# Optimization experiments

Measured on AMD Instinct MI355X. Metric: run time of the kernel, lower is better.

Reference implementation:

```python
import jax, jax.numpy as jnp
import numpy as np

VOCAB_SIZE = 128
HIDDEN_DIM = 128
NUM_STATES = 64
STACK_VOCAB_SIZE = 32
STACK_DEPTH = 64
NUM_MEM_ACTIONS = 2 + STACK_VOCAB_SIZE  # 0=NOOP, 1=POP, k>=2 => PUSH symbol (k-2)
NUM_BUF_ACTIONS = VOCAB_SIZE
T, B = 512, 512


def setup_inputs() -> dict:
    key = jax.random.key(0)
    ks = jax.random.split(key, 10)
    return {
        "x": jax.random.randint(ks[0], (T, B), 0, VOCAB_SIZE),
        "true_act": jax.random.randint(ks[1], (T, B), 0, NUM_MEM_ACTIONS),
        "true_s": jax.random.randint(ks[2], (T, B), 0, NUM_STATES),
        "use_forcing": jax.random.randint(ks[3], (T, B), 0, 2),
        "embed": jax.random.normal(ks[4], (VOCAB_SIZE, HIDDEN_DIM), jnp.float32) * 0.02,
        "W_mem": jax.random.normal(ks[5], (HIDDEN_DIM + NUM_STATES + STACK_VOCAB_SIZE, NUM_MEM_ACTIONS), jnp.float32) * 0.05,
        "b_mem": jnp.zeros((NUM_MEM_ACTIONS,), jnp.float32),
        "W_buf": jax.random.normal(ks[6], (HIDDEN_DIM + NUM_STATES + STACK_VOCAB_SIZE, NUM_BUF_ACTIONS), jnp.float32) * 0.05,
        "b_buf": jnp.zeros((NUM_BUF_ACTIONS,), jnp.float32),
        "W_state": jax.random.normal(ks[7], (HIDDEN_DIM + NUM_STATES + STACK_VOCAB_SIZE, NUM_STATES), jnp.float32) * 0.05,
        "b_state": jnp.zeros((NUM_STATES,), jnp.float32),
    }


def update_stack(stack, ptr, action):
    # stack: [STACK_DEPTH] int, ptr: [] int, action: [] int
    is_push = action >= 2
    is_pop = action == 1
    new_ptr = jnp.clip(ptr + jnp.where(is_push, 1, 0) - jnp.where(is_pop, 1, 0), 0, STACK_DEPTH - 1)
    sym = jnp.maximum(action - 2, 0)
    stack_new = stack.at[new_ptr].set(jnp.where(is_push, sym, stack[new_ptr]))
    r_new = stack_new[new_ptr]  # read top of stack
    return stack_new, new_ptr, r_new


def reference(x, true_act, true_s, use_forcing, embed, W_mem, b_mem, W_buf, b_buf, W_state, b_state):
    def step(carry, inp):
        stack, ptr, r_prev, s_prev = carry
        x_t, t_act, t_s, forcing = inp
        x_emb = embed[x_t]                                   # [B, H] gather
        s_emb = jax.nn.one_hot(s_prev, NUM_STATES, dtype=embed.dtype)
        r_emb = jax.nn.one_hot(r_prev, STACK_VOCAB_SIZE, dtype=embed.dtype)
        flat = jnp.concatenate([x_emb, s_emb, r_emb], axis=-1)  # [B, 224]
        logits_mem = flat @ W_mem + b_mem
        logits_buf = flat @ W_buf + b_buf
        logits_state = flat @ W_state + b_state
        pred_act = jnp.argmax(logits_mem, axis=-1)
        pred_state = jnp.argmax(logits_state, axis=-1)
        action = jnp.where(forcing > 0, t_act, pred_act)
        next_s = jnp.where(forcing > 0, t_s, pred_state)
        stack_new, ptr_new, r_new = jax.vmap(update_stack)(stack, ptr, action)
        return (stack_new, ptr_new, r_new, next_s), (logits_mem, logits_buf, logits_state)

    init = (
        jnp.zeros((B, STACK_DEPTH), jnp.int32),
        jnp.zeros((B,), jnp.int32),
        jnp.zeros((B,), jnp.int32),
        jnp.zeros((B,), jnp.int32),
    )
    _, (lm, lb, ls) = jax.lax.scan(step, init, (x, true_act, true_s, use_forcing))
    return lm, lb, ls
```

## Files before the change

kernel.cpp:

```cpp
#include <hip/hip_runtime.h>
#include <stdint.h>
#include <limits.h>


#define TT 512
#define BB 512
#define HH 128
#define NSs 64
#define NMm 34
#define NBb 128

typedef unsigned short u16;
typedef float f2 __attribute__((ext_vector_type(2)));

__global__ __launch_bounds__(256) void precompute_M(
    const float* __restrict__ embed,
    const float* __restrict__ Wm, const float* __restrict__ bm,
    const float* __restrict__ Wb, const float* __restrict__ bb,
    const float* __restrict__ Ws, const float* __restrict__ bs,
    float* __restrict__ Mm32, float* __restrict__ Ms32,
    float* __restrict__ Mb32, float* __restrict__ MmT,
    float* __restrict__ MsT) {
  __shared__ double e[HH];
  const int v = blockIdx.x;
  const int tid = threadIdx.x;
  if (tid < HH) e[tid] = (double)embed[v * HH + tid];
  __syncthreads();
  if (tid < NMm) {
    const int j = tid;
    double acc = 0.0;
    for (int h = 0; h < HH; ++h) acc += e[h] * (double)Wm[h * NMm + j];
    const float r = (float)(acc + (double)bm[j]);
    Mm32[v * NMm + j] = r;
    MmT[j * 128 + v] = r;
  } else if (tid < NMm + NSs) {
    const int j = tid - NMm;
    double acc = 0.0;
    for (int h = 0; h < HH; ++h) acc += e[h] * (double)Ws[h * NSs + j];
    const float r = (float)(acc + (double)bs[j]);
    Ms32[v * NSs + j] = r;
    MsT[j * 128 + v] = r;
  } else if (tid < NMm + NSs + NBb) {
    const int j = tid - NMm - NSs;
    double acc = 0.0;
    for (int h = 0; h < HH; ++h) acc += e[h] * (double)Wb[h * NBb + j];
    Mb32[v * NBb + j] = (float)(acc + (double)bb[j]);
  }
}

__global__ __launch_bounds__(128) void build_lut(
    const float* __restrict__ Wm, const float* __restrict__ Ws,
    const float* __restrict__ MmT, const float* __restrict__ MsT,
    u16* __restrict__ lut) {
  __shared__ float wms[NMm], wmr[NMm], wss[NSs], wsr[NSs];
  const int s = blockIdx.x >> 5;
  const int r = blockIdx.x & 31;
  const int tid = threadIdx.x;
  if (tid < NMm) {
    wms[tid] = Wm[(128 + s) * NMm + tid];
    wmr[tid] = Wm[(192 + r) * NMm + tid];
  }
  if (tid < NSs) {
    wss[tid] = Ws[(128 + s) * NSs + tid];
    wsr[tid] = Ws[(192 + r) * NSs + tid];
  }
  __syncthreads();

  const int v = tid;
  int bestm = INT_MIN, act = 0;
#pragma unroll
  for (int j = 0; j < NMm; ++j) {
    const double val = (double)MmT[j * 128 + v] + (double)wms[j] + (double)wmr[j];
    const int iv = (int)(val * 67108864.0);
    if (iv > bestm) { bestm = iv; act = j; }
  }
  int bests = INT_MIN, ns = 0;
#pragma unroll
  for (int j = 0; j < NSs; ++j) {
    const double val = (double)MsT[j * 128 + v] + (double)wss[j] + (double)wsr[j];
    const int iv = (int)(val * 67108864.0);
    if (iv > bests) { bests = iv; ns = j; }
  }
  lut[(unsigned)blockIdx.x * 128 + v] = (u16)(act | (ns << 6));
}

__global__ __launch_bounds__(512, 1) void sm_fused(
    const int* __restrict__ x, const int* __restrict__ tact,
    const int* __restrict__ tstate, const int* __restrict__ forc,
    const u16* __restrict__ lut,
    const float* __restrict__ Wm, const float* __restrict__ Wb,
    const float* __restrict__ Ws,
    const float* __restrict__ Mm32, const float* __restrict__ Ms32,
    const float* __restrict__ Mb32, float* __restrict__ out) {
  __shared__ unsigned sPk[TT];
  __shared__ volatile u16 trajL[TT];
  const int tid = threadIdx.x;
  const int b = blockIdx.x;
  for (int t = tid; t < TT; t += 512) {
    const int g = t * BB + b;
    sPk[t] = (unsigned)x[g] | ((unsigned)tact[g] << 8) |
             ((unsigned)tstate[g] << 16) | ((unsigned)forc[g] << 24);
    trajL[t] = 0xFFFFu;
  }
  __syncthreads();

  const int lane = tid & 63;
  const int w = tid >> 6;

  if (w == 0) {
    __builtin_amdgcn_s_setprio(1);
    int stackv = 0;
    int ptr = 0, rr = 0, s = 0;
    unsigned p0 = sPk[0], p1 = sPk[1], p2 = sPk[2];

    for (int t = 0; t < TT; ++t) {
      const unsigned p3 = sPk[t + 3 < TT ? t + 3 : TT - 1];
      const unsigned pk_s = __builtin_amdgcn_readfirstlane(p0);

      if (lane == 0) trajL[t] = (u16)(s | (rr << 8));

      int act, ns;
      if (pk_s >> 24) {
        act = (int)((p0 >> 8) & 63u);
        ns = (int)((p0 >> 16) & 63u);
      } else {
        const int idx = s * 4096 + rr * 128 + (int)(p0 & 127u);
        const int lv = lut[idx];
        act = lv & 63;
        ns = (lv >> 6) & 63;
      }

      const bool ispush = act >= 2;
      int npn = ptr + (ispush ? 1 : 0) - (act == 1 ? 1 : 0);
      npn = npn < 0 ? 0 : (npn > 63 ? 63 : npn);
      if (ispush && lane == npn) stackv = act - 2;
      rr = __builtin_amdgcn_ds_bpermute(npn * 4, stackv);
      ptr = npn;
      s = ns;

      p0 = p1; p1 = p2; p2 = p3;
    }
  } else {
    const int j = w - 1;
    float* outLM = out;
    float* outLB = out + (size_t)TT * BB * NMm;
    float* outLS = out + (size_t)TT * BB * (NMm + NBb);

    for (int t = j; t < TT; t += 7) {
      int pr = trajL[t];
      while (pr == 0xFFFF) {
        __builtin_amdgcn_s_sleep(4);
        pr = trajL[t];
      }
      const unsigned pk = sPk[t];
      const int xv = (int)(pk & 127u);
      const int s = pr & 255;
      const int r = pr >> 8;
      const int rs = 128 + s, rr = 192 + r;
      const int row = t * BB + b;
      if (lane < NMm)
        __builtin_nontemporal_store(
            Mm32[xv * NMm + lane] + Wm[rs * NMm + lane] + Wm[rr * NMm + lane],
            &outLM[(size_t)row * NMm + lane]);
      __builtin_nontemporal_store(
          Ms32[xv * NSs + lane] + Ws[rs * NSs + lane] + Ws[rr * NSs + lane],
          &outLS[(size_t)row * NSs + lane]);
      const f2 mb  = *(const f2*)&Mb32[xv * NBb + 2 * lane];
      const f2 wbs = *(const f2*)&Wb[rs * NBb + 2 * lane];
      const f2 wbr = *(const f2*)&Wb[rr * NBb + 2 * lane];
      f2 o;
      o.x = mb.x + wbs.x + wbr.x;
      o.y = mb.y + wbs.y + wbr.y;
      __builtin_nontemporal_store(o, (f2*)&outLB[(size_t)row * NBb + 2 * lane]);
    }
  }
}

extern "C" void kernel_launch(void* const* d_in, const int* in_sizes, int n_in,
                              void* d_out, int out_size, void* d_ws, size_t ws_size,
                              hipStream_t stream) {
  if (ws_size < 690176) return;

  const int* x     = (const int*)d_in[0];
  const int* tactp = (const int*)d_in[1];
  const int* tstp  = (const int*)d_in[2];
  const int* forcp = (const int*)d_in[3];
  const float* embed = (const float*)d_in[4];
  const float* Wm = (const float*)d_in[5];
  const float* bm = (const float*)d_in[6];
  const float* Wb = (const float*)d_in[7];
  const float* bb = (const float*)d_in[8];
  const float* Ws = (const float*)d_in[9];
  const float* bs = (const float*)d_in[10];

  char* wsp = (char*)d_ws;
  float* Mm32 = (float*)(wsp);
  float* Ms32 = (float*)(wsp + 17408);
  float* Mb32 = (float*)(wsp + 50176);
  float* MmT  = (float*)(wsp + 115712);
  float* MsT  = (float*)(wsp + 133120);
  u16*   lut  = (u16*)(wsp + 165888);

  precompute_M<<<128, 256, 0, stream>>>(embed, Wm, bm, Wb, bb, Ws, bs,
                                        Mm32, Ms32, Mb32, MmT, MsT);
  build_lut<<<2048, 128, 0, stream>>>(Wm, Ws, MmT, MsT, lut);
  sm_fused<<<512, 512, 0, stream>>>(x, tactp, tstp, forcp, lut,
                                    Wm, Wb, Ws, Mm32, Ms32, Mb32,
                                    (float*)d_out);
}
```

Before: 152.0 us.

## Keep stack as scalar bitplanes and stream packed inputs via readlane

The serial scan wave now stores the 64-deep stack as five 64-bit bitplanes in scalar registers instead of one lane-distributed value read back with ds_bpermute. Packed per-step inputs are preloaded into eight registers and extracted with readlane, which removes per-step LDS loads, and the LUT entries are widened to 32-bit and made uniform via readfirstlane. The goal is a shorter serial dependency chain per timestep by keeping the recurrence on the scalar unit. In exchange the LUT doubles in size and the workspace requirement grows, and the bitplane updates add extra scalar ALU work.

```diff
diff --git a/kernel.cpp b/kernel.cpp
--- a/kernel.cpp
+++ b/kernel.cpp
@@ -11,6 +11,7 @@
 #define NBb 128
 
 typedef unsigned short u16;
+typedef unsigned long long u64;
 typedef float f2 __attribute__((ext_vector_type(2)));
 
 __global__ __launch_bounds__(256) void precompute_M(
@@ -51,7 +52,7 @@
 __global__ __launch_bounds__(128) void build_lut(
     const float* __restrict__ Wm, const float* __restrict__ Ws,
     const float* __restrict__ MmT, const float* __restrict__ MsT,
-    u16* __restrict__ lut) {
+    unsigned* __restrict__ lut) {
   __shared__ float wms[NMm], wmr[NMm], wss[NSs], wsr[NSs];
   const int s = blockIdx.x >> 5;
   const int r = blockIdx.x & 31;
@@ -81,13 +82,13 @@
     const int iv = (int)(val * 67108864.0);
     if (iv > bests) { bests = iv; ns = j; }
   }
-  lut[(unsigned)blockIdx.x * 128 + v] = (u16)(act | (ns << 6));
+  lut[(unsigned)blockIdx.x * 128 + v] = (unsigned)(act | (ns << 6));
 }
 
 __global__ __launch_bounds__(512, 1) void sm_fused(
     const int* __restrict__ x, const int* __restrict__ tact,
     const int* __restrict__ tstate, const int* __restrict__ forc,
-    const u16* __restrict__ lut,
+    const unsigned* __restrict__ lut,
     const float* __restrict__ Wm, const float* __restrict__ Wb,
     const float* __restrict__ Ws,
     const float* __restrict__ Mm32, const float* __restrict__ Ms32,
@@ -109,36 +110,56 @@
 
   if (w == 0) {
     __builtin_amdgcn_s_setprio(1);
-    int stackv = 0;
+    unsigned pk0 = sPk[0 * 64 + lane], pk1 = sPk[1 * 64 + lane];
+    unsigned pk2 = sPk[2 * 64 + lane], pk3 = sPk[3 * 64 + lane];
+    unsigned pk4 = sPk[4 * 64 + lane], pk5 = sPk[5 * 64 + lane];
+    unsigned pk6 = sPk[6 * 64 + lane], pk7 = sPk[7 * 64 + lane];
+
+    u64 pl0 = 0, pl1 = 0, pl2 = 0, pl3 = 0, pl4 = 0;
     int ptr = 0, rr = 0, s = 0;
-    unsigned p0 = sPk[0], p1 = sPk[1], p2 = sPk[2];
-
-    for (int t = 0; t < TT; ++t) {
-      const unsigned p3 = sPk[t + 3 < TT ? t + 3 : TT - 1];
-      const unsigned pk_s = __builtin_amdgcn_readfirstlane(p0);
-
-      if (lane == 0) trajL[t] = (u16)(s | (rr << 8));
-
-      int act, ns;
-      if (pk_s >> 24) {
-        act = (int)((p0 >> 8) & 63u);
-        ns = (int)((p0 >> 16) & 63u);
-      } else {
-        const int idx = s * 4096 + rr * 128 + (int)(p0 & 127u);
-        const int lv = lut[idx];
-        act = lv & 63;
-        ns = (lv >> 6) & 63;
+
+#pragma unroll
+    for (int g2 = 0; g2 < 8; ++g2) {
+      const unsigned preg = (g2 == 0) ? pk0 : (g2 == 1) ? pk1
+                          : (g2 == 2) ? pk2 : (g2 == 3) ? pk3
+                          : (g2 == 4) ? pk4 : (g2 == 5) ? pk5
+                          : (g2 == 6) ? pk6 : pk7;
+      for (int t2 = 0; t2 < 64; ++t2) {
+        const int t = g2 * 64 + t2;
+        const unsigned pk =
+            (unsigned)__builtin_amdgcn_readlane((int)preg, t2);
+
+        if (lane == 0) trajL[t] = (u16)(s | (rr << 8));
+
+        int act, ns;
+        if (pk >> 24) {
+          act = (int)((pk >> 8) & 63u);
+          ns = (int)((pk >> 16) & 63u);
+        } else {
+          const int idx = s * 4096 + rr * 128 + (int)(pk & 127u);
+          const int lv = __builtin_amdgcn_readfirstlane((int)lut[idx]);
+          act = lv & 63;
+          ns = (lv >> 6) & 63;
+        }
+
+        const bool ispush = act >= 2;
+        int npn = ptr + (ispush ? 1 : 0) - (act == 1 ? 1 : 0);
+        npn = npn < 0 ? 0 : (npn > 63 ? 63 : npn);
+        if (ispush) {
+          const unsigned sym = (unsigned)(act - 2);
+          const u64 m = ~(1ULL << npn);
+          pl0 = (pl0 & m) | ((u64)(sym & 1u) << npn);
+          pl1 = (pl1 & m) | ((u64)((sym >> 1) & 1u) << npn);
+          pl2 = (pl2 & m) | ((u64)((sym >> 2) & 1u) << npn);
+          pl3 = (pl3 & m) | ((u64)((sym >> 3) & 1u) << npn);
+          pl4 = (pl4 & m) | ((u64)((sym >> 4) & 1u) << npn);
+        }
+        rr = (int)(((pl0 >> npn) & 1) | (((pl1 >> npn) & 1) << 1) |
+                   (((pl2 >> npn) & 1) << 2) | (((pl3 >> npn) & 1) << 3) |
+                   (((pl4 >> npn) & 1) << 4));
+        ptr = npn;
+        s = ns;
       }
-
-      const bool ispush = act >= 2;
-      int npn = ptr + (ispush ? 1 : 0) - (act == 1 ? 1 : 0);
-      npn = npn < 0 ? 0 : (npn > 63 ? 63 : npn);
-      if (ispush && lane == npn) stackv = act - 2;
-      rr = __builtin_amdgcn_ds_bpermute(npn * 4, stackv);
-      ptr = npn;
-      s = ns;
-
-      p0 = p1; p1 = p2; p2 = p3;
     }
   } else {
     const int j = w - 1;
@@ -179,7 +200,7 @@
 extern "C" void kernel_launch(void* const* d_in, const int* in_sizes, int n_in,
                               void* d_out, int out_size, void* d_ws, size_t ws_size,
                               hipStream_t stream) {
-  if (ws_size < 690176) return;
+  if (ws_size < 1214464) return;
 
   const int* x     = (const int*)d_in[0];
   const int* tactp = (const int*)d_in[1];
@@ -199,7 +220,7 @@
   float* Mb32 = (float*)(wsp + 50176);
   float* MmT  = (float*)(wsp + 115712);
   float* MsT  = (float*)(wsp + 133120);
-  u16*   lut  = (u16*)(wsp + 165888);
+  unsigned* lut = (unsigned*)(wsp + 165888);
 
   precompute_M<<<128, 256, 0, stream>>>(embed, Wm, bm, Wb, bb, Ws, bs,
                                         Mm32, Ms32, Mb32, MmT, MsT);
```

Result: slower. 193.1 us (+27.1%).
